# Optimization experiments

Measured on AMD Instinct MI355X. Metric: run time of the kernel, lower is better.

Reference implementation:

```python
import jax, jax.numpy as jnp
import numpy as np

B, L, H = 8, 192, 768


def setup_inputs() -> dict:
    key = jax.random.key(0)
    k1, k2, k3 = jax.random.split(key, 3)
    seq_hiddens = jax.random.normal(k1, (B, L, H), dtype=jnp.float32)
    # torch nn.Linear(2H, H): weight (H, 2H), bias (H,)
    W = jax.random.normal(k2, (H, 2 * H), dtype=jnp.float32) * (1.0 / np.sqrt(2 * H))
    b = jax.random.normal(k3, (H,), dtype=jnp.float32) * 0.01
    return {"seq_hiddens": seq_hiddens, "W": W, "b": b}


def reference(seq_hiddens, W, b):
    # Upper-triangular pair indices, row-major: for i in range(L): for j in range(i, L)
    L_ = seq_hiddens.shape[1]
    ii, jj = np.triu_indices(L_)  # static, each (P,) with P = L*(L+1)/2
    repeat_h = seq_hiddens[:, ii, :]   # [B, P, H] anchor token i repeated
    visible_h = seq_hiddens[:, jj, :]  # [B, P, H] token j >= i
    shaking = jnp.concatenate([repeat_h, visible_h], axis=-1)  # [B, P, 2H]
    out = jnp.tanh(jnp.einsum('bpk,hk->bph', shaking, W) + b)  # [B, P, H]
    return out
```

## Files before the change

### kernel.cpp

```cpp
#include <hip/hip_runtime.h>
#include <math.h>

#define L_SEQ 192
#define H_DIM 768
#define B_SZ  8
#define NPAIR (L_SEQ * (L_SEQ + 1) / 2)
#define MROWS (B_SZ * L_SEQ)
#define NCOLS (2 * H_DIM)

typedef short  bf16x8  __attribute__((ext_vector_type(8)));
typedef float  f32x4   __attribute__((ext_vector_type(4)));
typedef unsigned short u16x4 __attribute__((ext_vector_type(4)));

__device__ __forceinline__ void pair_from_p(int p, int& io, int& jo) {
    float tl = 2.0f * L_SEQ + 1.0f;
    int i = (int)((tl - sqrtf(tl * tl - 8.0f * (float)p)) * 0.5f);
    if (i < 0) i = 0;
    if (i > L_SEQ - 1) i = L_SEQ - 1;
    while (i > 0 && i * (2 * L_SEQ - i + 1) / 2 > p) --i;
    while (i < L_SEQ - 1 && (i + 1) * (2 * L_SEQ - i) / 2 <= p) ++i;
    io = i;
    jo = i + (p - i * (2 * L_SEQ - i + 1) / 2);
}

struct HL { unsigned short h, l; };

__device__ __forceinline__ HL split_bf16(float x) {
    HL r;
    unsigned u  = __float_as_uint(x);
    unsigned rh = u + 0x7FFFu + ((u >> 16) & 1u);
    r.h = (unsigned short)(rh >> 16);
    float hf = __uint_as_float((unsigned)r.h << 16);
    float res = x - hf;
    unsigned u2 = __float_as_uint(res);
    unsigned rl = u2 + 0x7FFFu + ((u2 >> 16) & 1u);
    r.l = (unsigned short)(rl >> 16);
    return r;
}

__device__ __forceinline__ float fast_tanh(float x) {
    float e = __builtin_amdgcn_exp2f(x * 2.885390081777927f);
    return 1.0f - 2.0f * __builtin_amdgcn_rcpf(e + 1.0f);
}

#define LDSP 40

__global__ __launch_bounds__(256) void gemm_mfma_kernel(
    const float* __restrict__ seq,
    const float* __restrict__ W,
    float* __restrict__ D)
{
    __shared__ unsigned short Ah[128 * LDSP], Al[128 * LDSP];
    __shared__ unsigned short Bh[128 * LDSP], Bl[128 * LDSP];

    const int t    = threadIdx.x;
    const int bn0  = blockIdx.x * 128;
    const int bm0  = blockIdx.y * 128;
    const int side = (bn0 >= H_DIM) ? 1 : 0;
    const int wrow0 = bn0 - side * H_DIM;
    const int kofs  = side * H_DIM;

    const int lane = t & 63;
    const int wave = t >> 6;
    const int wr   = wave >> 1, wc = wave & 1;
    const int l15  = lane & 15;
    const int kc   = (lane >> 4) * 8;

    const int sr = t >> 1;
    const int sk = (t & 1) * 16;

    f32x4 acc[4][4];
    #pragma unroll
    for (int a = 0; a < 4; ++a)
        #pragma unroll
        for (int b = 0; b < 4; ++b) acc[a][b] = (f32x4){0.f, 0.f, 0.f, 0.f};

    for (int k0 = 0; k0 < H_DIM; k0 += 32) {
        {
            const float* src = seq + (size_t)(bm0 + sr) * H_DIM + k0 + sk;
            unsigned short* dh = Ah + sr * LDSP + sk;
            unsigned short* dl = Al + sr * LDSP + sk;
            #pragma unroll
            for (int c = 0; c < 4; ++c) {
                float4 v = *reinterpret_cast<const float4*>(src + c * 4);
                HL sx = split_bf16(v.x), sy = split_bf16(v.y);
                HL sz = split_bf16(v.z), sw = split_bf16(v.w);
                u16x4 h = {sx.h, sy.h, sz.h, sw.h};
                u16x4 l = {sx.l, sy.l, sz.l, sw.l};
                *reinterpret_cast<u16x4*>(dh + c * 4) = h;
                *reinterpret_cast<u16x4*>(dl + c * 4) = l;
            }
        }
        {
            const float* src = W + (size_t)(wrow0 + sr) * NCOLS + kofs + k0 + sk;
            unsigned short* dh = Bh + sr * LDSP + sk;
            unsigned short* dl = Bl + sr * LDSP + sk;
            #pragma unroll
            for (int c = 0; c < 4; ++c) {
                float4 v = *reinterpret_cast<const float4*>(src + c * 4);
                HL sx = split_bf16(v.x), sy = split_bf16(v.y);
                HL sz = split_bf16(v.z), sw = split_bf16(v.w);
                u16x4 h = {sx.h, sy.h, sz.h, sw.h};
                u16x4 l = {sx.l, sy.l, sz.l, sw.l};
                *reinterpret_cast<u16x4*>(dh + c * 4) = h;
                *reinterpret_cast<u16x4*>(dl + c * 4) = l;
            }
        }
        __syncthreads();

        bf16x8 ah[4], al[4], bh[4], bl[4];
        #pragma unroll
        for (int mi = 0; mi < 4; ++mi) {
            int row = wr * 64 + mi * 16 + l15;
            ah[mi] = *reinterpret_cast<const bf16x8*>(Ah + row * LDSP + kc);
            al[mi] = *reinterpret_cast<const bf16x8*>(Al + row * LDSP + kc);
        }
        #pragma unroll
        for (int ni = 0; ni < 4; ++ni) {
            int row = wc * 64 + ni * 16 + l15;
            bh[ni] = *reinterpret_cast<const bf16x8*>(Bh + row * LDSP + kc);
            bl[ni] = *reinterpret_cast<const bf16x8*>(Bl + row * LDSP + kc);
        }

        #pragma unroll
        for (int mi = 0; mi < 4; ++mi)
            #pragma unroll
            for (int ni = 0; ni < 4; ++ni) {
                acc[mi][ni] = __builtin_amdgcn_mfma_f32_16x16x32_bf16(ah[mi], bh[ni], acc[mi][ni], 0, 0, 0);
                acc[mi][ni] = __builtin_amdgcn_mfma_f32_16x16x32_bf16(ah[mi], bl[ni], acc[mi][ni], 0, 0, 0);
                acc[mi][ni] = __builtin_amdgcn_mfma_f32_16x16x32_bf16(al[mi], bh[ni], acc[mi][ni], 0, 0, 0);
            }
        __syncthreads();
    }

    #pragma unroll
    for (int mi = 0; mi < 4; ++mi)
        #pragma unroll
        for (int ni = 0; ni < 4; ++ni) {
            int row0 = bm0 + wr * 64 + mi * 16 + (lane >> 4) * 4;
            int col  = bn0 + wc * 64 + ni * 16 + l15;
            #pragma unroll
            for (int r = 0; r < 4; ++r)
                D[(size_t)(row0 + r) * NCOLS + col] = acc[mi][ni][r];
        }
}

__global__ __launch_bounds__(192) void combine_kernel(
    const float* __restrict__ D,
    const float* __restrict__ bias,
    float* __restrict__ out)
{
    const int p = blockIdx.x;
    int i, j;
    pair_from_p(p, i, j);

    const int h = threadIdx.x * 4;
    const f32x4 bb = *reinterpret_cast<const f32x4*>(bias + h);

    #pragma unroll
    for (int b = 0; b < B_SZ; ++b) {
        const f32x4 a = *reinterpret_cast<const f32x4*>(D + (size_t)(b * L_SEQ + i) * NCOLS + h);
        const f32x4 c = *reinterpret_cast<const f32x4*>(D + (size_t)(b * L_SEQ + j) * NCOLS + H_DIM + h);
        f32x4 o;
        o.x = fast_tanh(a.x + c.x + bb.x);
        o.y = fast_tanh(a.y + c.y + bb.y);
        o.z = fast_tanh(a.z + c.z + bb.z);
        o.w = fast_tanh(a.w + c.w + bb.w);
        __builtin_nontemporal_store(o, reinterpret_cast<f32x4*>(out + ((size_t)b * NPAIR + p) * H_DIM + h));
    }
}

__global__ __launch_bounds__(256) void naive_kernel(
    const float* __restrict__ seq,
    const float* __restrict__ W,
    const float* __restrict__ bias,
    float* __restrict__ out)
{
    const int p = blockIdx.x;
    const int b = blockIdx.y;
    int i, j;
    pair_from_p(p, i, j);
    const float* si = seq + ((size_t)b * L_SEQ + i) * H_DIM;
    const float* sj = seq + ((size_t)b * L_SEQ + j) * H_DIM;
    for (int h = threadIdx.x; h < H_DIM; h += 256) {
        const float* wr = W + (size_t)h * NCOLS;
        float s = bias[h];
        for (int k = 0; k < H_DIM; ++k)
            s += si[k] * wr[k] + sj[k] * wr[H_DIM + k];
        out[((size_t)b * NPAIR + p) * H_DIM + h] = tanhf(s);
    }
}

extern "C" void kernel_launch(void* const* d_in, const int* in_sizes, int n_in,
                              void* d_out, int out_size, void* d_ws, size_t ws_size,
                              hipStream_t stream) {
    const float* seq  = (const float*)d_in[0];
    const float* W    = (const float*)d_in[1];
    const float* bias = (const float*)d_in[2];
    float* out = (float*)d_out;

    const size_t need = (size_t)MROWS * NCOLS * sizeof(float);
    if (ws_size >= need) {
        float* D = (float*)d_ws;
        dim3 g1(NCOLS / 128, MROWS / 128);
        hipLaunchKernelGGL(gemm_mfma_kernel, g1, dim3(256), 0, stream, seq, W, D);
        hipLaunchKernelGGL(combine_kernel, dim3(NPAIR), dim3(192), 0, stream, D, bias, out);
    } else {
        dim3 g(NPAIR, B_SZ);
        hipLaunchKernelGGL(naive_kernel, g, dim3(256), 0, stream, seq, W, bias, out);
    }
}
```

Baseline: 137.6 us.

## Tile combine kernel over 8x8 pair blocks to reuse projected rows

```diff
diff --git a/kernel.cpp b/kernel.cpp
--- a/kernel.cpp
+++ b/kernel.cpp
@@ -7,20 +7,22 @@
 #define NPAIR (L_SEQ * (L_SEQ + 1) / 2)
 #define MROWS (B_SZ * L_SEQ)
 #define NCOLS (2 * H_DIM)
+#define NTILE 24
+#define NTRI  (NTILE * (NTILE + 1) / 2)
 
 typedef short  bf16x8  __attribute__((ext_vector_type(8)));
 typedef float  f32x4   __attribute__((ext_vector_type(4)));
 typedef unsigned short u16x4 __attribute__((ext_vector_type(4)));
 
-__device__ __forceinline__ void pair_from_p(int p, int& io, int& jo) {
-    float tl = 2.0f * L_SEQ + 1.0f;
+__device__ __forceinline__ void tri_decode(int p, int Lq, int& io, int& jo) {
+    float tl = 2.0f * Lq + 1.0f;
     int i = (int)((tl - sqrtf(tl * tl - 8.0f * (float)p)) * 0.5f);
     if (i < 0) i = 0;
-    if (i > L_SEQ - 1) i = L_SEQ - 1;
-    while (i > 0 && i * (2 * L_SEQ - i + 1) / 2 > p) --i;
-    while (i < L_SEQ - 1 && (i + 1) * (2 * L_SEQ - i) / 2 <= p) ++i;
+    if (i > Lq - 1) i = Lq - 1;
+    while (i > 0 && i * (2 * Lq - i + 1) / 2 > p) --i;
+    while (i < Lq - 1 && (i + 1) * (2 * Lq - i) / 2 <= p) ++i;
     io = i;
-    jo = i + (p - i * (2 * L_SEQ - i + 1) / 2);
+    jo = i + (p - i * (2 * Lq - i + 1) / 2);
 }
 
 struct HL { unsigned short h, l; };
@@ -145,28 +147,46 @@
         }
 }
 
-__global__ __launch_bounds__(192) void combine_kernel(
+__global__ __launch_bounds__(192) void combine_tile_kernel(
     const float* __restrict__ D,
     const float* __restrict__ bias,
     float* __restrict__ out)
 {
-    const int p = blockIdx.x;
-    int i, j;
-    pair_from_p(p, i, j);
+    const int b = blockIdx.y;
+    int it, jt;
+    tri_decode(blockIdx.x, NTILE, it, jt);
 
     const int h = threadIdx.x * 4;
     const f32x4 bb = *reinterpret_cast<const f32x4*>(bias + h);
-
-    #pragma unroll
-    for (int b = 0; b < B_SZ; ++b) {
-        const f32x4 a = *reinterpret_cast<const f32x4*>(D + (size_t)(b * L_SEQ + i) * NCOLS + h);
-        const f32x4 c = *reinterpret_cast<const f32x4*>(D + (size_t)(b * L_SEQ + j) * NCOLS + H_DIM + h);
-        f32x4 o;
-        o.x = fast_tanh(a.x + c.x + bb.x);
-        o.y = fast_tanh(a.y + c.y + bb.y);
-        o.z = fast_tanh(a.z + c.z + bb.z);
-        o.w = fast_tanh(a.w + c.w + bb.w);
-        __builtin_nontemporal_store(o, reinterpret_cast<f32x4*>(out + ((size_t)b * NPAIR + p) * H_DIM + h));
+    const float* Dbase = D + (size_t)b * L_SEQ * NCOLS;
+
+    f32x4 Ar[8], Cr[8];
+    #pragma unroll
+    for (int r = 0; r < 8; ++r)
+        Ar[r] = *reinterpret_cast<const f32x4*>(Dbase + (size_t)(it * 8 + r) * NCOLS + h) + bb;
+    #pragma unroll
+    for (int r = 0; r < 8; ++r)
+        Cr[r] = *reinterpret_cast<const f32x4*>(Dbase + (size_t)(jt * 8 + r) * NCOLS + H_DIM + h);
+
+    const int diag = (it == jt);
+
+    #pragma unroll
+    for (int di = 0; di < 8; ++di) {
+        const int i = it * 8 + di;
+        const int prow = i * (2 * L_SEQ - i + 1) / 2 - i;
+        float* orow = out + ((size_t)b * NPAIR + prow) * H_DIM + h;
+        #pragma unroll
+        for (int dj = 0; dj < 8; ++dj) {
+            if (diag && dj < di) continue;
+            const int j = jt * 8 + dj;
+            f32x4 s = Ar[di] + Cr[dj];
+            f32x4 o;
+            o.x = fast_tanh(s.x);
+            o.y = fast_tanh(s.y);
+            o.z = fast_tanh(s.z);
+            o.w = fast_tanh(s.w);
+            __builtin_nontemporal_store(o, reinterpret_cast<f32x4*>(orow + (size_t)j * H_DIM));
+        }
     }
 }
 
@@ -179,7 +199,7 @@
     const int p = blockIdx.x;
     const int b = blockIdx.y;
     int i, j;
-    pair_from_p(p, i, j);
+    tri_decode(p, L_SEQ, i, j);
     const float* si = seq + ((size_t)b * L_SEQ + i) * H_DIM;
     const float* sj = seq + ((size_t)b * L_SEQ + j) * H_DIM;
     for (int h = threadIdx.x; h < H_DIM; h += 256) {
@@ -204,7 +224,8 @@
         float* D = (float*)d_ws;
         dim3 g1(NCOLS / 128, MROWS / 128);
         hipLaunchKernelGGL(gemm_mfma_kernel, g1, dim3(256), 0, stream, seq, W, D);
-        hipLaunchKernelGGL(combine_kernel, dim3(NPAIR), dim3(192), 0, stream, D, bias, out);
+        dim3 g2(NTRI, B_SZ);
+        hipLaunchKernelGGL(combine_tile_kernel, g2, dim3(192), 0, stream, D, bias, out);
     } else {
         dim3 g(NPAIR, B_SZ);
         hipLaunchKernelGGL(naive_kernel, g, dim3(256), 0, stream, seq, W, bias, out);
```

Result: no change. 138.5 us (+0.6%).
